# Optimization experiments

Hardware: AMD Instinct MI355X
Metric: run time of the kernel (lower is better)

Reference implementation:

```python
import jax, jax.numpy as jnp
import numpy as np
from jax import lax

B, T, V, D, H, C = 256, 1024, 5000, 100, 64, 2


def setup_inputs() -> dict:
    key = jax.random.key(0)
    k0, k1, k2, k3, k4 = jax.random.split(key, 5)
    tokens = jax.random.randint(k0, (B, T), 0, V)  # 0 is the mask/pad id
    E = jax.random.normal(k1, (V, D), dtype=jnp.float32) * 0.05
    W = jax.random.normal(k2, (D, H), dtype=jnp.float32) * (1.0 / np.sqrt(D))
    U = jax.random.normal(k3, (H, H), dtype=jnp.float32) * (1.0 / np.sqrt(H))
    b = jnp.zeros((H,), dtype=jnp.float32)
    Wd = jax.random.normal(k4, (H, C), dtype=jnp.float32) * (1.0 / np.sqrt(H))
    bd = jnp.zeros((C,), dtype=jnp.float32)
    return {"tokens": tokens, "E": E, "W": W, "U": U, "b": b, "Wd": Wd, "bd": bd}


def reference(tokens, E, W, U, b, Wd, bd):
    # Embedding with mask_zero=True: mask where token != 0
    x = E[tokens]                      # [B, T, D]
    mask = tokens != 0                 # [B, T] bool
    # Precompute input projection for all timesteps (batched GEMM).
    xW = jnp.einsum('btd,dh->bth', x, W) + b  # [B, T, H]

    def step(h, inp):
        xw_t, m_t = inp                # xw_t: [B,H], m_t: [B]
        h_new = jnp.tanh(xw_t + h @ U)
        # Keras masked recurrence: masked steps carry previous state/output.
        h = jnp.where(m_t[:, None], h_new, h)
        return h, h

    h0 = jnp.zeros((tokens.shape[0], U.shape[0]), dtype=xW.dtype)
    _, hs = lax.scan(step, h0, (jnp.swapaxes(xW, 0, 1), mask.T))  # hs: [T, B, H]
    hs = jnp.swapaxes(hs, 0, 1)        # [B, T, H]
    pooled = jnp.mean(hs, axis=1)      # tf.reduce_mean over time (unmasked mean)
    # Dropout is identity at inference.
    logits = pooled @ Wd + bd
    return jax.nn.sigmoid(logits)
```

## Files before the change

### kernel.cpp

```cpp
#include <hip/hip_runtime.h>

#define B_ 256
#define T_ 1024
#define V_ 5000
#define D_ 100
#define H_ 64
#define C_ 2

typedef float f32x4 __attribute__((ext_vector_type(4)));

__global__ __launch_bounds__(256) void ew_kernel(const float* __restrict__ E,
                                                 const float* __restrict__ W,
                                                 const float* __restrict__ bias,
                                                 float* __restrict__ EW) {
    int idx = blockIdx.x * 256 + threadIdx.x;
    if (idx >= V_ * H_) return;
    int h = idx & (H_ - 1);
    int v = idx >> 6;
    float acc = bias[h];
    const float* Erow = E + v * D_;
    #pragma unroll 4
    for (int d = 0; d < D_; ++d) {
        acc = fmaf(Erow[d], W[d * H_ + h], acc);
    }
    EW[idx] = 2.0f * acc;
}

__global__ __launch_bounds__(64, 1) void rnn_kernel(const int* __restrict__ tokens,
                                                    const float* __restrict__ EW,
                                                    const float* __restrict__ U,
                                                    const float* __restrict__ Wd,
                                                    const float* __restrict__ bd,
                                                    float* __restrict__ out) {
    const int b = blockIdx.x;
    const int j = threadIdx.x;

    __shared__ int   sh_tok[T_ + 2];
    __shared__ float sh_h[H_];

    f32x4 uq[16];
    #pragma unroll
    for (int c = 0; c < 16; ++c) {
        uq[c][0] = 2.0f * U[(4 * c + 0) * H_ + j];
        uq[c][1] = 2.0f * U[(4 * c + 1) * H_ + j];
        uq[c][2] = 2.0f * U[(4 * c + 2) * H_ + j];
        uq[c][3] = 2.0f * U[(4 * c + 3) * H_ + j];
    }
    asm volatile("" : "+v"(uq[0]), "+v"(uq[1]), "+v"(uq[2]), "+v"(uq[3]),
                      "+v"(uq[4]), "+v"(uq[5]), "+v"(uq[6]), "+v"(uq[7]),
                      "+v"(uq[8]), "+v"(uq[9]), "+v"(uq[10]), "+v"(uq[11]),
                      "+v"(uq[12]), "+v"(uq[13]), "+v"(uq[14]), "+v"(uq[15]));

    const int* tok = tokens + b * T_;
    #pragma unroll
    for (int k = 0; k < T_ / H_; ++k) {
        sh_tok[k * H_ + j] = tok[k * H_ + j];
    }
    if (j < 2) sh_tok[T_ + j] = 0;
    __syncthreads();

    float h = 0.f;
    float pooled = 0.f;

    int2 tkA = *(const int2*)&sh_tok[0];
    float xw0 = EW[tkA.x * H_ + j];
    float xw1 = EW[tkA.y * H_ + j];

    #define RNN_STEP(tokv, xwv)                                          \
    {                                                                    \
        sh_h[j] = h;                                                     \
        float a0 = (xwv), a1 = 0.f, a2 = 0.f, a3 = 0.f;                  \
        _Pragma("unroll")                                                \
        for (int c = 0; c < 16; ++c) {                                   \
            f32x4 hv = *(const f32x4*)&sh_h[4 * c];                      \
            a0 = fmaf(hv[0], uq[c][0], a0);                              \
            a1 = fmaf(hv[1], uq[c][1], a1);                              \
            a2 = fmaf(hv[2], uq[c][2], a2);                              \
            a3 = fmaf(hv[3], uq[c][3], a3);                              \
        }                                                                \
        float x2 = (a0 + a1) + (a2 + a3);                                \
        float e = __expf(x2);                                            \
        float r = __builtin_amdgcn_rcpf(e + 1.f);                        \
        float hn = fmaf(-2.f, r, 1.f);                                   \
        h = ((tokv) != 0) ? hn : h;                                      \
        pooled += h;                                                     \
    }

    for (int t = 0; t < T_; t += 2) {
        asm volatile("" :: "v"(uq[0]), "v"(uq[1]), "v"(uq[2]), "v"(uq[3]),
                           "v"(uq[4]), "v"(uq[5]), "v"(uq[6]), "v"(uq[7]),
                           "v"(uq[8]), "v"(uq[9]), "v"(uq[10]), "v"(uq[11]),
                           "v"(uq[12]), "v"(uq[13]), "v"(uq[14]), "v"(uq[15]));

        int2 tkB = *(const int2*)&sh_tok[t + 2];
        float xw2 = EW[tkB.x * H_ + j];
        float xw3 = EW[tkB.y * H_ + j];

        RNN_STEP(tkA.x, xw0);
        RNN_STEP(tkA.y, xw1);

        tkA = tkB;
        xw0 = xw2;
        xw1 = xw3;
    }
    #undef RNN_STEP

    float p = pooled * (1.0f / (float)T_);
    float v0 = p * Wd[j * C_ + 0];
    float v1 = p * Wd[j * C_ + 1];
    #pragma unroll
    for (int off = 32; off >= 1; off >>= 1) {
        v0 += __shfl_down(v0, off, 64);
        v1 += __shfl_down(v1, off, 64);
    }
    if (j == 0) {
        float l0 = v0 + bd[0];
        float l1 = v1 + bd[1];
        out[b * C_ + 0] = 1.f / (1.f + __expf(-l0));
        out[b * C_ + 1] = 1.f / (1.f + __expf(-l1));
    }
}

extern "C" void kernel_launch(void* const* d_in, const int* in_sizes, int n_in,
                              void* d_out, int out_size, void* d_ws, size_t ws_size,
                              hipStream_t stream) {
    const int*   tokens = (const int*)  d_in[0];
    const float* E      = (const float*)d_in[1];
    const float* W      = (const float*)d_in[2];
    const float* U      = (const float*)d_in[3];
    const float* bias   = (const float*)d_in[4];
    const float* Wd     = (const float*)d_in[5];
    const float* bd     = (const float*)d_in[6];
    float* out = (float*)d_out;
    float* EW  = (float*)d_ws;

    ew_kernel<<<(V_ * H_ + 255) / 256, 256, 0, stream>>>(E, W, bias, EW);
    rnn_kernel<<<B_, H_, 0, stream>>>(tokens, EW, U, Wd, bd, out);
}
```

Measured before the change: 349.2 us.

## Interleave four batch sequences per wavefront in RNN kernel

Each workgroup now handles four batch elements, interleaving their recurrence steps so independent dependency chains hide LDS, FMA and transcendental latency. The grid shrinks from 256 to 64 single-wave blocks, so fewer compute units are used and per-wave instruction count grows. The bet is that the serial step latency, not throughput, dominated the old kernel.

After: 1.207 ms. +245.6%, slower.

```diff
diff --git a/kernel.cpp b/kernel.cpp
--- a/kernel.cpp
+++ b/kernel.cpp
@@ -6,6 +6,7 @@
 #define D_ 100
 #define H_ 64
 #define C_ 2
+#define NE_ 4
 
 typedef float f32x4 __attribute__((ext_vector_type(4)));
 
@@ -32,11 +33,11 @@
                                                     const float* __restrict__ Wd,
                                                     const float* __restrict__ bd,
                                                     float* __restrict__ out) {
-    const int b = blockIdx.x;
-    const int j = threadIdx.x;
+    const int b0 = blockIdx.x * NE_;
+    const int j  = threadIdx.x;
 
-    __shared__ int   sh_tok[T_ + 2];
-    __shared__ float sh_h[H_];
+    __shared__ int   sh_tok[NE_][T_ + 2];
+    __shared__ float sh_h[NE_][H_];
 
     f32x4 uq[16];
     #pragma unroll
@@ -51,39 +52,47 @@
                       "+v"(uq[8]), "+v"(uq[9]), "+v"(uq[10]), "+v"(uq[11]),
                       "+v"(uq[12]), "+v"(uq[13]), "+v"(uq[14]), "+v"(uq[15]));
 
-    const int* tok = tokens + b * T_;
     #pragma unroll
-    for (int k = 0; k < T_ / H_; ++k) {
-        sh_tok[k * H_ + j] = tok[k * H_ + j];
+    for (int e = 0; e < NE_; ++e) {
+        const int* tok = tokens + (b0 + e) * T_;
+        #pragma unroll
+        for (int k = 0; k < T_ / H_; ++k) {
+            sh_tok[e][k * H_ + j] = tok[k * H_ + j];
+        }
+        if (j < 2) sh_tok[e][T_ + j] = 0;
     }
-    if (j < 2) sh_tok[T_ + j] = 0;
     __syncthreads();
 
-    float h = 0.f;
-    float pooled = 0.f;
+    float h[NE_], pooled[NE_];
+    int2  tkA[NE_];
+    float xw0[NE_], xw1[NE_];
+    #pragma unroll
+    for (int e = 0; e < NE_; ++e) {
+        h[e] = 0.f;
+        pooled[e] = 0.f;
+        tkA[e] = *(const int2*)&sh_tok[e][0];
+        xw0[e] = EW[tkA[e].x * H_ + j];
+        xw1[e] = EW[tkA[e].y * H_ + j];
+    }
 
-    int2 tkA = *(const int2*)&sh_tok[0];
-    float xw0 = EW[tkA.x * H_ + j];
-    float xw1 = EW[tkA.y * H_ + j];
-
-    #define RNN_STEP(tokv, xwv)                                          \
+    #define RNN_STEP(e, tokv, xwv)                                       \
     {                                                                    \
-        sh_h[j] = h;                                                     \
+        sh_h[e][j] = h[e];                                               \
         float a0 = (xwv), a1 = 0.f, a2 = 0.f, a3 = 0.f;                  \
         _Pragma("unroll")                                                \
         for (int c = 0; c < 16; ++c) {                                   \
-            f32x4 hv = *(const f32x4*)&sh_h[4 * c];                      \
+            f32x4 hv = *(const f32x4*)&sh_h[e][4 * c];                   \
             a0 = fmaf(hv[0], uq[c][0], a0);                              \
             a1 = fmaf(hv[1], uq[c][1], a1);                              \
             a2 = fmaf(hv[2], uq[c][2], a2);                              \
             a3 = fmaf(hv[3], uq[c][3], a3);                              \
         }                                                                \
         float x2 = (a0 + a1) + (a2 + a3);                                \
-        float e = __expf(x2);                                            \
-        float r = __builtin_amdgcn_rcpf(e + 1.f);                        \
+        float ef = __expf(x2);                                           \
+        float r = __builtin_amdgcn_rcpf(ef + 1.f);                       \
         float hn = fmaf(-2.f, r, 1.f);                                   \
-        h = ((tokv) != 0) ? hn : h;                                      \
-        pooled += h;                                                     \
+        h[e] = ((tokv) != 0) ? hn : h[e];                                \
+        pooled[e] += h[e];                                               \
     }
 
     for (int t = 0; t < T_; t += 2) {
@@ -92,32 +101,47 @@
                            "v"(uq[8]), "v"(uq[9]), "v"(uq[10]), "v"(uq[11]),
                            "v"(uq[12]), "v"(uq[13]), "v"(uq[14]), "v"(uq[15]));
 
-        int2 tkB = *(const int2*)&sh_tok[t + 2];
-        float xw2 = EW[tkB.x * H_ + j];
-        float xw3 = EW[tkB.y * H_ + j];
+        int2  tkB[NE_];
+        float xw2[NE_], xw3[NE_];
+        #pragma unroll
+        for (int e = 0; e < NE_; ++e) {
+            tkB[e] = *(const int2*)&sh_tok[e][t + 2];
+            xw2[e] = EW[tkB[e].x * H_ + j];
+            xw3[e] = EW[tkB[e].y * H_ + j];
+        }
 
-        RNN_STEP(tkA.x, xw0);
-        RNN_STEP(tkA.y, xw1);
+        #pragma unroll
+        for (int e = 0; e < NE_; ++e) RNN_STEP(e, tkA[e].x, xw0[e]);
+        #pragma unroll
+        for (int e = 0; e < NE_; ++e) RNN_STEP(e, tkA[e].y, xw1[e]);
 
-        tkA = tkB;
-        xw0 = xw2;
-        xw1 = xw3;
+        #pragma unroll
+        for (int e = 0; e < NE_; ++e) {
+            tkA[e] = tkB[e];
+            xw0[e] = xw2[e];
+            xw1[e] = xw3[e];
+        }
     }
     #undef RNN_STEP
 
-    float p = pooled * (1.0f / (float)T_);
-    float v0 = p * Wd[j * C_ + 0];
-    float v1 = p * Wd[j * C_ + 1];
+    float wd0 = Wd[j * C_ + 0];
+    float wd1 = Wd[j * C_ + 1];
     #pragma unroll
-    for (int off = 32; off >= 1; off >>= 1) {
-        v0 += __shfl_down(v0, off, 64);
-        v1 += __shfl_down(v1, off, 64);
-    }
-    if (j == 0) {
-        float l0 = v0 + bd[0];
-        float l1 = v1 + bd[1];
-        out[b * C_ + 0] = 1.f / (1.f + __expf(-l0));
-        out[b * C_ + 1] = 1.f / (1.f + __expf(-l1));
+    for (int e = 0; e < NE_; ++e) {
+        float p = pooled[e] * (1.0f / (float)T_);
+        float v0 = p * wd0;
+        float v1 = p * wd1;
+        #pragma unroll
+        for (int off = 32; off >= 1; off >>= 1) {
+            v0 += __shfl_down(v0, off, 64);
+            v1 += __shfl_down(v1, off, 64);
+        }
+        if (j == 0) {
+            float l0 = v0 + bd[0];
+            float l1 = v1 + bd[1];
+            out[(b0 + e) * C_ + 0] = 1.f / (1.f + __expf(-l0));
+            out[(b0 + e) * C_ + 1] = 1.f / (1.f + __expf(-l1));
+        }
     }
 }
 
@@ -135,5 +159,5 @@
     float* EW  = (float*)d_ws;
 
     ew_kernel<<<(V_ * H_ + 255) / 256, 256, 0, stream>>>(E, W, bias, EW);
-    rnn_kernel<<<B_, H_, 0, stream>>>(tokens, EW, U, Wd, bd, out);
+    rnn_kernel<<<B_ / NE_, H_, 0, stream>>>(tokens, EW, U, Wd, bd, out);
 }
```
